# Optimization experiments

Hardware: AMD Instinct MI355X
Metric: run time of the kernel (lower is better)

Reference implementation:

```python
import jax, jax.numpy as jnp
import numpy as np

EPS = 1.1920929e-07  # torch.finfo(float32).eps, default for F.rms_norm
HQ, HKV = 16, 4
WIN = 256

def rmsnorm(x):
    return x * jax.lax.rsqrt(jnp.mean(x * x, axis=-1, keepdims=True) + EPS)

def setup_inputs() -> dict:
    key = jax.random.key(0)
    ks = jax.random.split(key, 5)
    B, T, C = 2, 2048, 2048
    Dh = C // HQ
    s = 0.02
    x = jax.random.normal(ks[0], (B, T, C), jnp.float32)
    Wq = jax.random.normal(ks[1], (C, HQ * Dh), jnp.float32) * s
    Wk = jax.random.normal(ks[2], (C, HKV * Dh), jnp.float32) * s
    Wv = jax.random.normal(ks[3], (C, HKV * Dh), jnp.float32) * s
    Wo = jax.random.normal(ks[4], (C, C), jnp.float32) * s
    return {"x": x, "Wq": Wq, "Wk": Wk, "Wv": Wv, "Wo": Wo}

def reference(x, Wq, Wk, Wv, Wo):
    B, T, C = x.shape
    Dh = C // HQ
    g = HQ // HKV
    # projections (Linear bias=False); weights stored [in,out]
    Q = (x @ Wq).reshape(B, T, HQ, Dh).transpose(0, 2, 1, 3)   # [B,Hq,T,Dh]
    V = (x @ Wv).reshape(B, T, HKV, Dh).transpose(0, 2, 1, 3)  # [B,Hkv,T,Dh]
    _K_unused = x @ Wk  # source computes c_k(x) but then overwrites K = norm(V)
    Q = rmsnorm(Q)
    K = rmsnorm(V)  # faithful to source bug: K = norm(V)
    Q = Q.reshape(B, HKV, g, T, Dh)
    scores = jnp.einsum('bhgtd,bhsd->bhgts', Q, K)  # no 1/sqrt(Dh) scale, as in source
    i = jnp.arange(T)[:, None]
    j = jnp.arange(T)[None, :]
    mask = (j > i) & (j <= i - WIN)
    scores = jnp.where(mask, -jnp.inf, scores)
    p = jax.nn.softmax(scores, axis=-1)
    y = jnp.einsum('bhgts,bhsd->bhgtd', p, V)
    y = y.reshape(B, HQ, T, Dh).transpose(0, 2, 1, 3).reshape(B, T, C)
    return rmsnorm(y @ Wo)
```

## Files before the change

### kernel.cpp

```cpp
#include <hip/hip_runtime.h>
#include <math.h>

#define BB   2
#define TT   2048
#define CC   2048
#define HQ_  16
#define HKV_ 4
#define DH   128
#define MM   (BB * TT)
#define KVC  (HKV_ * DH)

typedef __attribute__((ext_vector_type(8)))  _Float16 f16x8;
typedef __attribute__((ext_vector_type(4)))  float    f32x4;

__device__ __forceinline__ unsigned short f2h(float x) {
    _Float16 h = (_Float16)x;
    return __builtin_bit_cast(unsigned short, h);
}
__device__ __forceinline__ float h2f(unsigned short u) {
    return (float)__builtin_bit_cast(_Float16, u);
}
__device__ __forceinline__ void gll16(const void* g, void* l) {
    __builtin_amdgcn_global_load_lds(
        (const __attribute__((address_space(1))) unsigned int*)g,
        (__attribute__((address_space(3))) unsigned int*)l, 16, 0, 0);
}
__device__ __forceinline__ int xcd_swizzle(int lid, int nwg) {
    const int xcd = lid & 7, rank = lid >> 3;
    const int q8 = nwg >> 3, r8 = nwg & 7;
    return (xcd < r8 ? xcd * (q8 + 1) : r8 * (q8 + 1) + (xcd - r8) * q8) + rank;
}

__global__ __launch_bounds__(256)
void cast_f16(const float* __restrict__ in, unsigned short* __restrict__ out, int n8) {
    int i = blockIdx.x * blockDim.x + threadIdx.x;
    const int stride = gridDim.x * blockDim.x;
    for (; i < n8; i += stride) {
        const float4 a = ((const float4*)in)[i * 2 + 0];
        const float4 b = ((const float4*)in)[i * 2 + 1];
        uint4 o;
        o.x = (unsigned)f2h(a.x) | ((unsigned)f2h(a.y) << 16);
        o.y = (unsigned)f2h(a.z) | ((unsigned)f2h(a.w) << 16);
        o.z = (unsigned)f2h(b.x) | ((unsigned)f2h(b.y) << 16);
        o.w = (unsigned)f2h(b.z) | ((unsigned)f2h(b.w) << 16);
        ((uint4*)out)[i] = o;
    }
}

__global__ __launch_bounds__(256)
void tcast(const float* __restrict__ W, unsigned short* __restrict__ WT, int Kd, int Nd) {
    __shared__ float Ls[32][33];
    const int n0 = blockIdx.x * 32, k0 = blockIdx.y * 32;
    const int i = threadIdx.x;
    {
        const int kr = i >> 3, n4 = (i & 7) * 4;
        float4 v = *(const float4*)&W[(size_t)(k0 + kr) * Nd + n0 + n4];
        Ls[kr][n4 + 0] = v.x; Ls[kr][n4 + 1] = v.y;
        Ls[kr][n4 + 2] = v.z; Ls[kr][n4 + 3] = v.w;
    }
    __syncthreads();
    {
        const int nr = i >> 3, k4 = (i & 7) * 4;
        uint2 o;
        o.x = (unsigned)f2h(Ls[k4 + 0][nr]) | ((unsigned)f2h(Ls[k4 + 1][nr]) << 16);
        o.y = (unsigned)f2h(Ls[k4 + 2][nr]) | ((unsigned)f2h(Ls[k4 + 3][nr]) << 16);
        *(uint2*)&WT[(size_t)(n0 + nr) * Kd + k0 + k4] = o;
    }
}

template<int F16OUT>
__global__ __launch_bounds__(256)
void gemm_bt(const unsigned short* __restrict__ A, const unsigned short* __restrict__ Bt,
             void* __restrict__ Cout, int M, int N, int K) {
    __shared__ __align__(16) unsigned short As[128 * 64];
    __shared__ __align__(16) unsigned short Bs[128 * 64];
    const int tid  = threadIdx.x;
    const int lane = tid & 63, wid = tid >> 6;
    const int g = lane >> 4, l15 = lane & 15;
    const int nwg  = gridDim.x * gridDim.y;
    const int tile = xcd_swizzle(blockIdx.y * gridDim.x + blockIdx.x, nwg);
    const int bm = (tile / gridDim.x) * 128, bn = (tile % gridDim.x) * 128;
    const int wr = (wid >> 1) * 64, wc = (wid & 1) * 64;

    f32x4 acc[4][4] = {};

    for (int kt = 0; kt < K; kt += 64) {
        __syncthreads();
#pragma unroll
        for (int r = 0; r < 4; ++r) {
            const int q = r * 256 + tid;
            const int row = q >> 3, c = q & 7, sc = c ^ (row & 7);
            gll16(A + (size_t)(bm + row) * K + kt + sc * 8, As + q * 8);
        }
#pragma unroll
        for (int r = 0; r < 4; ++r) {
            const int q = r * 256 + tid;
            const int row = q >> 3, c = q & 7, sc = c ^ (row & 7);
            gll16(Bt + (size_t)(bn + row) * K + kt + sc * 8, Bs + q * 8);
        }
        __syncthreads();

#pragma unroll
        for (int kk = 0; kk < 2; ++kk) {
            f16x8 af[4], bfr[4];
#pragma unroll
            for (int m = 0; m < 4; ++m) {
                const int row = wr + m * 16 + l15;
                const int ch = (kk * 4 + g) ^ (row & 7);
                af[m] = *(const f16x8*)&As[row * 64 + ch * 8];
            }
#pragma unroll
            for (int n = 0; n < 4; ++n) {
                const int row = wc + n * 16 + l15;
                const int ch = (kk * 4 + g) ^ (row & 7);
                bfr[n] = *(const f16x8*)&Bs[row * 64 + ch * 8];
            }
#pragma unroll
            for (int m = 0; m < 4; ++m)
#pragma unroll
                for (int n = 0; n < 4; ++n)
                    acc[m][n] = __builtin_amdgcn_mfma_f32_16x16x32_f16(
                        af[m], bfr[n], acc[m][n], 0, 0, 0);
        }
    }

#pragma unroll
    for (int m = 0; m < 4; ++m)
#pragma unroll
        for (int n = 0; n < 4; ++n)
#pragma unroll
            for (int r = 0; r < 4; ++r) {
                const int row = bm + wr + m * 16 + g * 4 + r;
                const int col = bn + wc + n * 16 + l15;
                const float v = acc[m][n][r];
                if (F16OUT)
                    ((unsigned short*)Cout)[(size_t)row * N + col] = f2h(v);
                else
                    ((float*)Cout)[(size_t)row * N + col] = v;
            }
}

__global__ __launch_bounds__(256)
void rms128_h(const unsigned short* __restrict__ in, unsigned short* __restrict__ out,
              int nrows, float post) {
    const int row  = blockIdx.x * 4 + (threadIdx.x >> 6);
    const int lane = threadIdx.x & 63;
    if (row >= nrows) return;
    const unsigned u = *(const unsigned*)(in + (size_t)row * DH + lane * 2);
    const float a = h2f((unsigned short)(u & 0xffff));
    const float b = h2f((unsigned short)(u >> 16));
    float ss = a * a + b * b;
#pragma unroll
    for (int o = 32; o >= 1; o >>= 1) ss += __shfl_xor(ss, o);
    const float sc = rsqrtf(ss * (1.f / DH) + 1.1920929e-07f) * post;
    const unsigned ov = (unsigned)f2h(a * sc) | ((unsigned)f2h(b * sc) << 16);
    *(unsigned*)(out + (size_t)row * DH + lane * 2) = ov;
}

__global__ __launch_bounds__(256)
void vt_build(const unsigned short* __restrict__ Vg, unsigned short* __restrict__ Vt) {
    __shared__ unsigned short Ls[32][36];
    const int t0 = blockIdx.x * 32;
    const int d0 = blockIdx.y * 32;
    const int bh = blockIdx.z;
    const int b = bh >> 2, hk = bh & 3;
    const int i = threadIdx.x;
    {
        const int tr = i >> 3, d4 = (i & 7) * 4;
        const unsigned short* src = Vg + (size_t)(b * TT + t0 + tr) * KVC + hk * DH + d0 + d4;
        const unsigned u0 = *(const unsigned*)(src);
        const unsigned u1 = *(const unsigned*)(src + 2);
        Ls[tr][d4 + 0] = (unsigned short)(u0 & 0xffff);
        Ls[tr][d4 + 1] = (unsigned short)(u0 >> 16);
        Ls[tr][d4 + 2] = (unsigned short)(u1 & 0xffff);
        Ls[tr][d4 + 3] = (unsigned short)(u1 >> 16);
    }
    __syncthreads();
    {
        const int dr = i >> 3, t4 = (i & 7) * 4;
        unsigned short* dst = Vt + ((size_t)bh * DH + d0 + dr) * TT + t0 + t4;
        const unsigned o0 = (unsigned)Ls[t4 + 0][dr] | ((unsigned)Ls[t4 + 1][dr] << 16);
        const unsigned o1 = (unsigned)Ls[t4 + 2][dr] | ((unsigned)Ls[t4 + 3][dr] << 16);
        *(unsigned*)(dst)     = o0;
        *(unsigned*)(dst + 2) = o1;
    }
}

__global__ __launch_bounds__(256, 4)
void attn_mfma(const unsigned short* __restrict__ Qb, const unsigned short* __restrict__ Kb,
               const unsigned short* __restrict__ Vt, unsigned short* __restrict__ Yb) {
    __shared__ __align__(16) unsigned short Ks[2][32 * 128];
    __shared__ __align__(16) unsigned short Vs[2][128 * 32];
    __shared__ __align__(16) unsigned short Ps[4][16 * 32];

    const int tid  = threadIdx.x;
    const int lane = tid & 63, wid = tid >> 6;
    const int g = lane >> 4, l15 = lane & 15;
    const int q0 = blockIdx.x * 64;
    const int bh = blockIdx.y;
    const int b = bh >> 4, h = bh & 15, hk = h >> 2;

    const size_t kbase = (size_t)(b * TT) * KVC + hk * DH;
    const size_t vbase = (size_t)(b * HKV_ + hk) * DH * TT;

#define STAGE(buf, st)                                                         \
    do {                                                                       \
        _Pragma("unroll")                                                      \
        for (int r = 0; r < 2; ++r) {                                          \
            const int qq = r * 256 + tid;                                      \
            const int key = qq >> 4, c = qq & 15, sc = c ^ (key & 7);          \
            gll16(Kb + kbase + (size_t)((st) + key) * KVC + sc * 8,            \
                  &Ks[buf][qq * 8]);                                           \
        }                                                                      \
        _Pragma("unroll")                                                      \
        for (int r = 0; r < 2; ++r) {                                          \
            const int qq = r * 256 + tid;                                      \
            const int d = qq >> 2, c = qq & 3;                                 \
            const int sc = c ^ (d & 3) ^ ((d >> 2) & 3);                       \
            gll16(Vt + vbase + (size_t)d * TT + (st) + sc * 8,                 \
                  &Vs[buf][qq * 8]);                                           \
        }                                                                      \
    } while (0)

    STAGE(0, 0);

    f16x8 qf[4];
    {
        const unsigned short* qp =
            Qb + (size_t)(b * TT + q0 + wid * 16 + l15) * CC + h * DH + g * 8;
#pragma unroll
        for (int kk = 0; kk < 4; ++kk) qf[kk] = *(const f16x8*)(qp + kk * 32);
    }
    {
        float ss = 0.f;
#pragma unroll
        for (int kk = 0; kk < 4; ++kk)
#pragma unroll
            for (int j = 0; j < 8; ++j) { const float v = (float)qf[kk][j]; ss += v * v; }
        ss += __shfl_xor(ss, 16);
        ss += __shfl_xor(ss, 32);
        const float qsc = rsqrtf(ss * (1.f / DH) + 1.1920929e-07f) * 1.4426950408889634f;
#pragma unroll
        for (int kk = 0; kk < 4; ++kk)
#pragma unroll
            for (int j = 0; j < 8; ++j)
                qf[kk][j] = (_Float16)((float)qf[kk][j] * qsc);
    }

    f16x8 ones_b;
    {
        const _Float16 v = (l15 == 0) ? (_Float16)1.0f : (_Float16)0.0f;
#pragma unroll
        for (int j = 0; j < 8; ++j) ones_b[j] = v;
    }

    float mr[4];
    f32x4 acc[9] = {};
#pragma unroll
    for (int r = 0; r < 4; ++r) mr[r] = -3.0e38f;

    unsigned short* pw = Ps[wid];

    asm volatile("s_waitcnt vmcnt(0)" ::: "memory");
    __builtin_amdgcn_s_barrier();

    const int NT = TT / 32;
    for (int t = 0; t < NT; ++t) {
        const int cur = t & 1;
        if (t + 1 < NT) STAGE(cur ^ 1, (t + 1) * 32);

        const unsigned short* ksp = Ks[cur];
        const unsigned short* vsp = Vs[cur];

        f32x4 s[2] = {};
        __builtin_amdgcn_s_setprio(1);
#pragma unroll
        for (int kk = 0; kk < 4; ++kk)
#pragma unroll
            for (int n = 0; n < 2; ++n) {
                const int key = n * 16 + l15;
                const int ch = (kk * 4 + g) ^ (key & 7);
                const f16x8 kf = *(const f16x8*)&ksp[key * 128 + ch * 8];
                s[n] = __builtin_amdgcn_mfma_f32_16x16x32_f16(qf[kk], kf, s[n], 0, 0, 0);
            }
        __builtin_amdgcn_s_setprio(0);

        float m0[4];
        bool need = false;
#pragma unroll
        for (int r = 0; r < 4; ++r) {
            m0[r] = fmaxf(s[0][r], s[1][r]);
            need = need || (m0[r] > mr[r] + 8.f);
        }
        if (__any(need)) {
            float scale[4];
#pragma unroll
            for (int r = 0; r < 4; ++r) {
                float mx = m0[r];
#pragma unroll
                for (int o = 8; o >= 1; o >>= 1) mx = fmaxf(mx, __shfl_xor(mx, o));
                const float mn = fmaxf(mr[r], mx);
                scale[r] = __builtin_amdgcn_exp2f(mr[r] - mn);
                mr[r] = mn;
            }
#pragma unroll
            for (int f = 0; f < 9; ++f) {
                acc[f][0] *= scale[0]; acc[f][1] *= scale[1];
                acc[f][2] *= scale[2]; acc[f][3] *= scale[3];
            }
        }

#pragma unroll
        for (int n = 0; n < 2; ++n) {
            const int colc = n * 2 + (l15 >> 3);
            const int cel  = l15 & 7;
#pragma unroll
            for (int r = 0; r < 4; ++r) {
                const float p = __builtin_amdgcn_exp2f(s[n][r] - mr[r]);
                const int row = g * 4 + r;
                const int ch = colc ^ (row & 3) ^ g;
                pw[row * 32 + ch * 8 + cel] = f2h(p);
            }
        }

        __builtin_amdgcn_s_setprio(1);
        {
            const int ch = g ^ (l15 & 3) ^ ((l15 >> 2) & 3);
            const f16x8 pa = *(const f16x8*)&pw[l15 * 32 + ch * 8];
#pragma unroll
            for (int f = 0; f < 8; ++f) {
                const int dr = f * 16 + l15;
                const int vch = g ^ (dr & 3) ^ ((dr >> 2) & 3);
                const f16x8 vf = *(const f16x8*)&vsp[dr * 32 + vch * 8];
                acc[f] = __builtin_amdgcn_mfma_f32_16x16x32_f16(pa, vf, acc[f], 0, 0, 0);
            }
            acc[8] = __builtin_amdgcn_mfma_f32_16x16x32_f16(pa, ones_b, acc[8], 0, 0, 0);
        }
        __builtin_amdgcn_s_setprio(0);

        asm volatile("s_waitcnt vmcnt(0)" ::: "memory");
        __builtin_amdgcn_s_barrier();
    }
#undef STAGE

    float inv[4];
#pragma unroll
    for (int r = 0; r < 4; ++r) {
        const float l = __shfl(acc[8][r], lane & 48);
        inv[r] = 1.f / l;
    }
#pragma unroll
    for (int f = 0; f < 8; ++f)
#pragma unroll
        for (int r = 0; r < 4; ++r) {
            const int t = q0 + wid * 16 + g * 4 + r;
            const int col = h * DH + f * 16 + l15;
            Yb[(size_t)(b * TT + t) * CC + col] = f2h(acc[f][r] * inv[r]);
        }
}

__global__ __launch_bounds__(256)
void rms2048_inplace(float* __restrict__ d) {
    __shared__ float red[4];
    const int tid = threadIdx.x;
    float* p = d + (size_t)blockIdx.x * CC;
    float4 a = *(float4*)&p[tid * 8];
    float4 b = *(float4*)&p[tid * 8 + 4];
    float ss = a.x * a.x + a.y * a.y + a.z * a.z + a.w * a.w +
               b.x * b.x + b.y * b.y + b.z * b.z + b.w * b.w;
#pragma unroll
    for (int o = 32; o >= 1; o >>= 1) ss += __shfl_xor(ss, o);
    if ((tid & 63) == 0) red[tid >> 6] = ss;
    __syncthreads();
    const float tot = red[0] + red[1] + red[2] + red[3];
    const float sc = rsqrtf(tot * (1.f / CC) + 1.1920929e-07f);
    a.x *= sc; a.y *= sc; a.z *= sc; a.w *= sc;
    b.x *= sc; b.y *= sc; b.z *= sc; b.w *= sc;
    *(float4*)&p[tid * 8]     = a;
    *(float4*)&p[tid * 8 + 4] = b;
}

extern "C" void kernel_launch(void* const* d_in, const int* in_sizes, int n_in,
                              void* d_out, int out_size, void* d_ws, size_t ws_size,
                              hipStream_t stream) {
    const float* x  = (const float*)d_in[0];
    const float* Wq = (const float*)d_in[1];
    const float* Wv = (const float*)d_in[3];
    const float* Wo = (const float*)d_in[4];
    float* out = (float*)d_out;

    char* ws = (char*)d_ws;
    const size_t MB = 1024 * 1024;
    unsigned short* xb  = (unsigned short*)(ws);
    unsigned short* WqT = (unsigned short*)(ws + 16 * MB);
    unsigned short* WoT = WqT;
    unsigned short* WvT = (unsigned short*)(ws + 24 * MB);
    unsigned short* Qg  = (unsigned short*)(ws + 26 * MB);
    unsigned short* Vg  = (unsigned short*)(ws + 42 * MB);
    unsigned short* Kb  = (unsigned short*)(ws + 46 * MB);
    unsigned short* Vt  = (unsigned short*)(ws + 50 * MB);
    unsigned short* Yb  = (unsigned short*)(ws + 54 * MB);

    const dim3 blk(256);

    cast_f16<<<2048, blk, 0, stream>>>(x, xb, MM * CC / 8);
    tcast<<<dim3(CC / 32, CC / 32), blk, 0, stream>>>(Wq, WqT, CC, CC);
    tcast<<<dim3(KVC / 32, CC / 32), blk, 0, stream>>>(Wv, WvT, CC, KVC);

    gemm_bt<1><<<dim3(CC / 128, MM / 128), blk, 0, stream>>>(xb, WqT, Qg, MM, CC, CC);
    gemm_bt<1><<<dim3(KVC / 128, MM / 128), blk, 0, stream>>>(xb, WvT, Vg, MM, KVC, CC);

    tcast<<<dim3(CC / 32, CC / 32), blk, 0, stream>>>(Wo, WoT, CC, CC);

    rms128_h<<<MM * HKV_ / 4, blk, 0, stream>>>(Vg, Kb, MM * HKV_, 1.f);
    vt_build<<<dim3(TT / 32, DH / 32, BB * HKV_), blk, 0, stream>>>(Vg, Vt);

    attn_mfma<<<dim3(TT / 64, BB * HQ_), blk, 0, stream>>>(Qg, Kb, Vt, Yb);

    gemm_bt<0><<<dim3(CC / 128, MM / 128), blk, 0, stream>>>(Yb, WoT, out, MM, CC, CC);
    rms2048_inplace<<<MM, blk, 0, stream>>>(out);
}
```

Before: 288.7 us.

## Triple-buffer attention K/V staging and emit output GEMM in fp16 before RMSNorm

```diff
diff --git a/kernel.cpp b/kernel.cpp
--- a/kernel.cpp
+++ b/kernel.cpp
@@ -186,11 +186,11 @@
     }
 }
 
-__global__ __launch_bounds__(256, 4)
+__global__ __launch_bounds__(256, 3)
 void attn_mfma(const unsigned short* __restrict__ Qb, const unsigned short* __restrict__ Kb,
                const unsigned short* __restrict__ Vt, unsigned short* __restrict__ Yb) {
-    __shared__ __align__(16) unsigned short Ks[2][32 * 128];
-    __shared__ __align__(16) unsigned short Vs[2][128 * 32];
+    __shared__ __align__(16) unsigned short Ks[3][32 * 128];
+    __shared__ __align__(16) unsigned short Vs[3][128 * 32];
     __shared__ __align__(16) unsigned short Ps[4][16 * 32];
 
     const int tid  = threadIdx.x;
@@ -223,6 +223,7 @@
     } while (0)
 
     STAGE(0, 0);
+    STAGE(1, 32);
 
     f16x8 qf[4];
     {
@@ -261,13 +262,14 @@
 
     unsigned short* pw = Ps[wid];
 
-    asm volatile("s_waitcnt vmcnt(0)" ::: "memory");
+    asm volatile("s_waitcnt vmcnt(8)" ::: "memory");
     __builtin_amdgcn_s_barrier();
 
     const int NT = TT / 32;
+    int cur = 0;
     for (int t = 0; t < NT; ++t) {
-        const int cur = t & 1;
-        if (t + 1 < NT) STAGE(cur ^ 1, (t + 1) * 32);
+        const int sb = (cur == 0) ? 2 : cur - 1;
+        if (t + 2 < NT) STAGE(sb, (t + 2) * 32);
 
         const unsigned short* ksp = Ks[cur];
         const unsigned short* vsp = Vs[cur];
@@ -338,8 +340,13 @@
         }
         __builtin_amdgcn_s_setprio(0);
 
-        asm volatile("s_waitcnt vmcnt(0)" ::: "memory");
+        if (t + 2 < NT) {
+            asm volatile("s_waitcnt vmcnt(8)" ::: "memory");
+        } else {
+            asm volatile("s_waitcnt vmcnt(0)" ::: "memory");
+        }
         __builtin_amdgcn_s_barrier();
+        cur = (cur == 2) ? 0 : cur + 1;
     }
 #undef STAGE
 
@@ -360,24 +367,28 @@
 }
 
 __global__ __launch_bounds__(256)
-void rms2048_inplace(float* __restrict__ d) {
+void rms2048_h(const unsigned short* __restrict__ in, float* __restrict__ out) {
     __shared__ float red[4];
     const int tid = threadIdx.x;
-    float* p = d + (size_t)blockIdx.x * CC;
-    float4 a = *(float4*)&p[tid * 8];
-    float4 b = *(float4*)&p[tid * 8 + 4];
-    float ss = a.x * a.x + a.y * a.y + a.z * a.z + a.w * a.w +
-               b.x * b.x + b.y * b.y + b.z * b.z + b.w * b.w;
+    const unsigned short* p = in + (size_t)blockIdx.x * CC + tid * 8;
+    const uint4 u = *(const uint4*)p;
+    float v[8];
+    v[0] = h2f((unsigned short)(u.x & 0xffff)); v[1] = h2f((unsigned short)(u.x >> 16));
+    v[2] = h2f((unsigned short)(u.y & 0xffff)); v[3] = h2f((unsigned short)(u.y >> 16));
+    v[4] = h2f((unsigned short)(u.z & 0xffff)); v[5] = h2f((unsigned short)(u.z >> 16));
+    v[6] = h2f((unsigned short)(u.w & 0xffff)); v[7] = h2f((unsigned short)(u.w >> 16));
+    float ss = 0.f;
+#pragma unroll
+    for (int j = 0; j < 8; ++j) ss += v[j] * v[j];
 #pragma unroll
     for (int o = 32; o >= 1; o >>= 1) ss += __shfl_xor(ss, o);
     if ((tid & 63) == 0) red[tid >> 6] = ss;
     __syncthreads();
     const float tot = red[0] + red[1] + red[2] + red[3];
     const float sc = rsqrtf(tot * (1.f / CC) + 1.1920929e-07f);
-    a.x *= sc; a.y *= sc; a.z *= sc; a.w *= sc;
-    b.x *= sc; b.y *= sc; b.z *= sc; b.w *= sc;
-    *(float4*)&p[tid * 8]     = a;
-    *(float4*)&p[tid * 8 + 4] = b;
+    float* q = out + (size_t)blockIdx.x * CC + tid * 8;
+    *(float4*)&q[0] = make_float4(v[0] * sc, v[1] * sc, v[2] * sc, v[3] * sc);
+    *(float4*)&q[4] = make_float4(v[4] * sc, v[5] * sc, v[6] * sc, v[7] * sc);
 }
 
 extern "C" void kernel_launch(void* const* d_in, const int* in_sizes, int n_in,
@@ -417,6 +428,6 @@
 
     attn_mfma<<<dim3(TT / 64, BB * HQ_), blk, 0, stream>>>(Qg, Kb, Vt, Yb);
 
-    gemm_bt<0><<<dim3(CC / 128, MM / 128), blk, 0, stream>>>(Yb, WoT, out, MM, CC, CC);
-    rms2048_inplace<<<MM, blk, 0, stream>>>(out);
-}
+    gemm_bt<1><<<dim3(CC / 128, MM / 128), blk, 0, stream>>>(Yb, WoT, xb, MM, CC, CC);
+    rms2048_h<<<MM, blk, 0, stream>>>(xb, out);
+}
```

Measured after the change: 319.5 us. +10.7%, slower.
